# Kernel tuning notes

Measured on AMD Instinct MI355X. Metric: run time of the kernel, lower is better.

## Reference

```python
import jax, jax.numpy as jnp
import numpy as np

EPS = 1e-5
NEG = -1e9

def _ln(x, g, b):
    m = x.mean(-1, keepdims=True)
    v = ((x - m) ** 2).mean(-1, keepdims=True)
    return (x - m) / jnp.sqrt(v + EPS) * g + b

def setup_inputs() -> dict:
    key = jax.random.key(0)
    ks = jax.random.split(key, 32)
    B, N, D, F, L = 2, 512, 128, 512, 3
    s = 0.05
    rn = lambda k, sh, sc=s: jax.random.normal(k, sh, jnp.float32) * sc
    inp = {
        'rel_matrix': rn(ks[0], (B, N, N, 2), 1.0),
        'pre_w': rn(ks[1], (2, D)), 'pre_b': rn(ks[2], (D,)),
        'proj_w': rn(ks[3], (2 * D, D)), 'proj_b': rn(ks[4], (D,)),
        'out_w1': rn(ks[5], (D, D)),
        'bn_g': 1.0 + rn(ks[6], (D,)), 'bn_b': rn(ks[7], (D,)),
        'bn_m': rn(ks[8], (D,)),
        'bn_v': 0.5 + jax.random.uniform(ks[9], (D,), jnp.float32),
        'out_w2': rn(ks[10], (D, D)), 'out_b2': rn(ks[11], (D,)),
        'pe': rn(ks[12], (128, D)),
        'wq': rn(ks[13], (L, D, D)), 'bq': rn(ks[14], (L, D)),
        'wk': rn(ks[15], (L, D, D)), 'bk': rn(ks[16], (L, D)),
        'wv': rn(ks[17], (L, D, D)), 'bv': rn(ks[18], (L, D)),
        'wo': rn(ks[19], (L, D, D)), 'bo': rn(ks[20], (L, D)),
        'ln1g': jnp.ones((L, D), jnp.float32), 'ln1b': jnp.zeros((L, D), jnp.float32),
        'ln2g': jnp.ones((L, D), jnp.float32), 'ln2b': jnp.zeros((L, D), jnp.float32),
        'fw1': rn(ks[21], (L, D, F)), 'fb1': rn(ks[22], (L, F)),
        'fw2': rn(ks[23], (L, F, D)), 'fb2': rn(ks[24], (L, D)),
        'mask': jax.random.randint(ks[25], (B, N), 0, 2) > 0,
        'agent_id': jax.random.randint(ks[26], (B, N), 0, 128, dtype=jnp.int32),
    }
    return inp

def reference(rel_matrix, pre_w, pre_b, proj_w, proj_b, out_w1, bn_g, bn_b, bn_m, bn_v,
              out_w2, out_b2, pe, wq, bq, wk, bk, wv, bv, wo, bo,
              ln1g, ln1b, ln2g, ln2b, fw1, fb1, fw2, fb2, mask, agent_id):
    # --- pairwise relation chain (the headroom target) ---
    # symmetric pairwise validity mask (B,N,N)
    pm = (mask[:, None, :] & mask[:, :, None]).astype(rel_matrix.dtype)
    count = jnp.maximum(pm.sum(axis=2), 1.0)  # (B,N) valid-partner counts
    x = rel_matrix @ pre_w + pre_b            # (B,N,N,D) pre_proj Linear(2->128)
    pooled = jnp.einsum('bijd,bij->bid', x, pm) / count[..., None]  # masked mean over j
    x = jnp.concatenate([x, jnp.broadcast_to(pooled[:, :, None, :], x.shape)], axis=-1)
    x = x @ proj_w + proj_b                   # Linear(256->128)
    x = jnp.einsum('bijd,bij->bid', x, pm) / count[..., None]       # masked mean over j
    # out MLP: Linear(no bias) + BatchNorm1d(eval) + ReLU + Linear
    h = x @ out_w1
    h = (h - bn_m) / jnp.sqrt(bn_v + EPS) * bn_g + bn_b
    x = jax.nn.relu(h) @ out_w2 + out_b2
    x = x + pe[agent_id]                      # agent positional embedding
    # --- 3 post-norm single-head transformer layers (eval, dropout off) ---
    kbias = jnp.where(mask, 0.0, NEG)[:, None, :]  # key padding bias (B,1,N)
    scale = 1.0 / jnp.sqrt(jnp.asarray(x.shape[-1], x.dtype))
    for l in range(3):
        q = x @ wq[l] + bq[l]
        k = x @ wk[l] + bk[l]
        v = x @ wv[l] + bv[l]
        a = jax.nn.softmax(jnp.einsum('bid,bjd->bij', q, k) * scale + kbias, axis=-1)
        att = jnp.einsum('bij,bjd->bid', a, v) @ wo[l] + bo[l]
        x = _ln(x + att, ln1g[l], ln1b[l])
        ff = jax.nn.relu(x @ fw1[l] + fb1[l]) @ fw2[l] + fb2[l]
        x = _ln(x + ff, ln2g[l], ln2b[l])
    return x
```

## Files before the change

### kernel.cpp

```cpp
#include <hip/hip_runtime.h>
#include <hip/hip_bf16.h>

typedef unsigned short u16;
typedef unsigned int u32;
typedef unsigned char u8;
typedef __attribute__((ext_vector_type(8))) short bf16x8;
typedef __attribute__((ext_vector_type(4))) float f32x4;

#define DEV __device__ __forceinline__

DEV float bf2f(u16 u) { union { u32 i; float f; } c; c.i = ((u32)u) << 16; return c.f; }
DEV u16 f2bf(float f) {
  union { float f; u32 i; } c; c.f = f;
  u32 r = c.i + 0x7FFFu + ((c.i >> 16) & 1u);
  return (u16)(r >> 16);
}
DEV u32 pk2(float lo, float hi) { return (u32)f2bf(lo) | ((u32)f2bf(hi) << 16); }
DEV float rdsrc(const void* p, int e, int isb) {
  return isb ? bf2f(((const u16*)p)[e]) : ((const float*)p)[e];
}
DEV bf16x8 as_bf(uint4 v) { union { uint4 u; bf16x8 h; } c; c.u = v; return c.h; }

static constexpr int B = 2, N = 512, D = 128, F = 512;
static constexpr int NROW = B * N;
static constexpr float EPS = 1e-5f;
static constexpr float NEG = -1e9f;
static constexpr float SCALE = 0.08838834764831845f;

#define OFF_PRE_W   0
#define OFF_PRE_B   256
#define OFF_PROJ_B  33152
#define OFF_BN_G    49664
#define OFF_BN_B    49792
#define OFF_BN_M    49920
#define OFF_BN_V    50048
#define OFF_OUT_B2  66560
#define OFF_PE      66688
#define OFF_BQ      132224
#define OFF_BK      181760
#define OFF_BV      231296
#define OFF_BO      280832
#define OFF_LN1G    281216
#define OFF_LN1B    281600
#define OFF_LN2G    281984
#define OFF_LN2B    282368
#define OFF_FB1     479360
#define OFF_FB2     677504
#define W_TOTAL     677888

static constexpr int PB_PROJ = 0;
static constexpr int PB_OW1  = 8192;
static constexpr int PB_OW2  = 16384;
static constexpr int PB_L0   = 24576;
static constexpr int PB_LSTR = 98304;
static constexpr int PB_WO   = 24576;
static constexpr int PB_FW1  = 32768;
static constexpr int PB_FW2  = 65536;
static constexpr int PTOT    = 79872;

struct NEnt { const void* s; int off, n; };
struct PEnt { const void* s1; const void* s2; int o1, o2, dst, lgn, cum; };
struct PrepArgs { NEnt nrm[19]; PEnt pk[21]; };

template<int KT>
DEV f32x4 mmaKo(const uint4* __restrict__ aPk, const uint4* __restrict__ Bp,
                int ncol, int col, int lane, int kt0) {
  f32x4 acc = {0.f, 0.f, 0.f, 0.f};
  const int sub = lane >> 4;
  #pragma unroll
  for (int kt = 0; kt < KT; ++kt) {
    const int e8 = (kt0 + kt) * 4 + sub;
    acc = __builtin_amdgcn_mfma_f32_16x16x32_bf16(
        as_bf(aPk[e8 * 16 + (lane & 15)]),
        as_bf(Bp[(size_t)e8 * ncol + col]),
        acc, 0, 0, 0);
  }
  return acc;
}

template<int KT>
DEV void loadB(const uint4* __restrict__ Bp, int ncol, int col, int lane,
               int kt0, uint4* breg) {
  const int sub = lane >> 4;
  #pragma unroll
  for (int kt = 0; kt < KT; ++kt)
    breg[kt] = Bp[(size_t)((kt0 + kt) * 4 + sub) * ncol + col];
}

template<int KT>
DEV f32x4 mmaR(const uint4* __restrict__ aPk, const uint4* breg, int lane, int kt0) {
  f32x4 acc = {0.f, 0.f, 0.f, 0.f};
  const int sub = lane >> 4;
  #pragma unroll
  for (int kt = 0; kt < KT; ++kt) {
    const int e8 = (kt0 + kt) * 4 + sub;
    acc = __builtin_amdgcn_mfma_f32_16x16x32_bf16(
        as_bf(aPk[e8 * 16 + (lane & 15)]),
        as_bf(breg[kt]),
        acc, 0, 0, 0);
  }
  return acc;
}

DEV void packRD(u32* aPkU, int r, int d, float v) {
  const float p = __shfl_xor(v, 1, 64);
  if (!(d & 1))
    aPkU[(((d >> 3) * 16 + r) << 2) + ((d >> 1) & 3)] = pk2(v, p);
}

DEV void packP16(u32* aPkU, int colbase, int lane, f32x4 v) {
  f32x4 p;
  #pragma unroll
  for (int g = 0; g < 4; ++g) p[g] = __shfl_xor(v[g], 1, 64);
  if (!(lane & 1)) {
    const int c = colbase + lane;
    const int e8 = c >> 3, slot = (c >> 1) & 3;
    #pragma unroll
    for (int g = 0; g < 4; ++g)
      aPkU[((e8 * 16 + g) << 2) + slot] = pk2(v[g], p[g]);
  }
}

__global__ __launch_bounds__(256) void k_prep(PrepArgs pa,
    const void* __restrict__ bnv, const void* __restrict__ maskp,
    int* __restrict__ flags, int* __restrict__ mbuf,
    float* __restrict__ W, u32* __restrict__ Wb)
{
  const int t = threadIdx.x, bid = blockIdx.x;
  __shared__ int s_nb, s_m4, s_m2;
  if (t == 0) { s_nb = 0; s_m4 = 0; s_m2 = 0; }
  __syncthreads();
  if (t < 64) {
    const u32 w = ((const u32*)bnv)[t];
    if (((w >> 8) & 0xFFu) != 0x3Fu || ((w >> 24) & 0xFFu) != 0x3Fu)
      atomicOr(&s_nb, 1);
  }
  __syncthreads();
  const int isb = s_nb ? 0 : 1;

  if (bid < 16) {
    for (int ten = 0; ten < 19; ++ten) {
      const NEnt E = pa.nrm[ten];
      for (int e = bid * 256 + t; e < E.n; e += 16 * 256)
        W[E.off + e] = rdsrc(E.s, e, isb);
    }
  } else if (bid < 511) {
    for (int g = (bid - 16) * 256 + t; g < PTOT; g += 495 * 256) {
      int ei = 0;
      #pragma unroll
      for (int k = 1; k < 21; ++k) if (g >= pa.pk[k].cum) ei = k;
      const PEnt E = pa.pk[ei];
      const int li = g - E.cum;
      const int e8 = li >> E.lgn, c = li & ((1 << E.lgn) - 1);
      float f[8];
      #pragma unroll
      for (int i = 0; i < 8; ++i) {
        const int si = ((e8 * 8 + i) << E.lgn) + c;
        f[i] = rdsrc(E.s1, E.o1 + si, isb);
        if (E.s2) f[i] += rdsrc(E.s2, E.o2 + si, isb);
      }
      uint4 w;
      w.x = pk2(f[0], f[1]); w.y = pk2(f[2], f[3]);
      w.z = pk2(f[4], f[5]); w.w = pk2(f[6], f[7]);
      ((uint4*)(Wb + E.dst))[li] = w;
    }
  } else {
    {
      const u32 w = ((const u32*)maskp)[t];
      if (!(w == 0u || w == 1u || w == 0x3F800000u)) atomicOr(&s_m4, 1);
      if (!(w == 0u || w == 1u || w == 0x10000u || w == 0x10001u ||
            w == 0x3F80u || w == 0x3F800000u || w == 0x3F803F80u)) atomicOr(&s_m2, 1);
    }
    __syncthreads();
    const int mode = (!s_m4) ? 4 : ((!s_m2) ? 2 : 1);
    if (t == 0) { flags[0] = isb; flags[1] = mode; }
    #pragma unroll
    for (int k = 0; k < 4; ++k) {
      const int e = k * 256 + t;
      int v;
      if (mode == 4)      v = (((const u32*)maskp)[e] != 0u);
      else if (mode == 2) v = (((const u16*)maskp)[e] != 0);
      else                v = (((const u8*)maskp)[e]  != 0);
      mbuf[e] = v;
    }
  }
}

__global__ __launch_bounds__(512) void k_relq(
    const void* __restrict__ relv, const float* __restrict__ W,
    const u32* __restrict__ Wb,
    const int* __restrict__ flags, const int* __restrict__ mbuf,
    const int* __restrict__ agent_id, float* __restrict__ xbuf,
    u32* __restrict__ qP, u32* __restrict__ kbT, u32* __restrict__ vbT)
{
  const int t = threadIdx.x;
  const int blk = blockIdx.x;
  const int row0 = blk * 4;
  const int b = row0 >> 9;
  const int wid = t >> 6;
  const int lane = t & 63;

  __shared__ uint4 aPk[2][256];
  __shared__ float wred[8][9];
  __shared__ float sT0[4], sT1[4], sMt;

  u32* a0 = (u32*)&aPk[0][0];
  u32* a1 = (u32*)&aPk[1][0];

  float s0[4] = {0, 0, 0, 0}, s1[4] = {0, 0, 0, 0}, cnt;
  {
    const int j = t;
    const float m = (float)mbuf[b * N + j];
    cnt = m;
    if (flags[0]) {
      const u32* rel2 = (const u32*)relv;
      #pragma unroll
      for (int r = 0; r < 4; ++r) {
        const u32 u = rel2[(size_t)(row0 + r) * N + j];
        s0[r] += m * bf2f((u16)(u & 0xFFFFu));
        s1[r] += m * bf2f((u16)(u >> 16));
      }
    } else {
      const float2* relf = (const float2*)relv;
      #pragma unroll
      for (int r = 0; r < 4; ++r) {
        const float2 u = relf[(size_t)(row0 + r) * N + j];
        s0[r] += m * u.x; s1[r] += m * u.y;
      }
    }
  }
  if ((t & 15) >= 4) {
    const uint4 z = {0u, 0u, 0u, 0u};
    aPk[t >> 8][t & 255] = z;
  }
  #pragma unroll
  for (int o = 32; o > 0; o >>= 1) {
    #pragma unroll
    for (int r = 0; r < 4; ++r) {
      s0[r] += __shfl_xor(s0[r], o, 64);
      s1[r] += __shfl_xor(s1[r], o, 64);
    }
    cnt += __shfl_xor(cnt, o, 64);
  }
  if ((t & 63) == 0) {
    #pragma unroll
    for (int r = 0; r < 4; ++r) { wred[wid][r] = s0[r]; wred[wid][4 + r] = s1[r]; }
    wred[wid][8] = cnt;
  }
  __syncthreads();
  if (t < 4) {
    float a0v = 0, a1v = 0;
    #pragma unroll
    for (int w = 0; w < 8; ++w) { a0v += wred[w][t]; a1v += wred[w][4 + t]; }
    sT0[t] = a0v; sT1[t] = a1v;
  }
  if (t == 8) {
    float c = 0;
    #pragma unroll
    for (int w = 0; w < 8; ++w) c += wred[w][8];
    sMt = c;
  }
  __syncthreads();

  {
    const int r = t >> 7, c = t & 127;
    const int mi = mbuf[row0 + r];
    const float v = mi ? (sT0[r] * W[OFF_PRE_W + c] + sT1[r] * W[OFF_PRE_W + D + c]) / sMt
                         + W[OFF_PRE_B + c]
                       : 0.f;
    packRD(a0, r, c, v);
  }
  __syncthreads();

  {
    const int col = wid * 16 + (lane & 15);
    f32x4 acc = mmaKo<4>(&aPk[0][0], (const uint4*)(Wb + PB_PROJ), 128, col, lane, 0);
    if (lane < 16) {
      const float pb = W[OFF_PROJ_B + col];
      f32x4 v;
      #pragma unroll
      for (int g = 0; g < 4; ++g) v[g] = mbuf[row0 + g] ? acc[g] + pb : 0.f;
      packP16(a1, wid * 16, lane, v);
    }
  }
  __syncthreads();

  {
    const int col = wid * 16 + (lane & 15);
    f32x4 acc = mmaKo<4>(&aPk[1][0], (const uint4*)(Wb + PB_OW1), 128, col, lane, 0);
    if (lane < 16) {
      const float bnm = W[OFF_BN_M + col];
      const float rs  = __frsqrt_rn(W[OFF_BN_V + col] + EPS);
      const float bg  = W[OFF_BN_G + col], bb = W[OFF_BN_B + col];
      f32x4 v;
      #pragma unroll
      for (int g = 0; g < 4; ++g) v[g] = fmaxf((acc[g] - bnm) * rs * bg + bb, 0.f);
      packP16(a0, wid * 16, lane, v);
    }
  }
  __syncthreads();

  {
    const int col = wid * 16 + (lane & 15);
    f32x4 acc = mmaKo<4>(&aPk[0][0], (const uint4*)(Wb + PB_OW2), 128, col, lane, 0);
    if (lane < 16) {
      const float ob = W[OFF_OUT_B2 + col];
      f32x4 v;
      #pragma unroll
      for (int g = 0; g < 4; ++g) {
        const int aid = agent_id[row0 + g];
        v[g] = acc[g] + ob + W[OFF_PE + aid * D + col];
        xbuf[(size_t)(row0 + g) * D + col] = v[g];
      }
      packP16(a1, wid * 16, lane, v);
    }
  }
  __syncthreads();

  {
    const int col = wid * 16 + (lane & 15);
    const int i0 = row0 & 511;
    #pragma unroll
    for (int m = 0; m < 3; ++m) {
      f32x4 acc = mmaKo<4>(&aPk[1][0], (const uint4*)(Wb + PB_L0 + m * 8192), 128, col, lane, 0);
      if (lane < 16) {
        const float bb = W[(m == 0 ? OFF_BQ : m == 1 ? OFF_BK : OFF_BV) + col];
        f32x4 v;
        #pragma unroll
        for (int g = 0; g < 4; ++g) v[g] = acc[g] + bb;
        if (m == 0) {
          f32x4 p;
          #pragma unroll
          for (int g = 0; g < 4; ++g) p[g] = __shfl_xor(v[g], 1, 64);
          if (!(lane & 1)) {
            const int e8 = col >> 3, slot = (col >> 1) & 3;
            #pragma unroll
            for (int g = 0; g < 4; ++g)
              qP[blk * 256 + (e8 * 4 + g) * 4 + slot] = pk2(v[g], p[g]);
          }
        } else if (m == 1) {
          f32x4 p;
          #pragma unroll
          for (int g = 0; g < 4; ++g) p[g] = __shfl_xor(v[g], 1, 64);
          if (!(lane & 1)) {
            const int e8 = col >> 3, slot = (col >> 1) & 3;
            #pragma unroll
            for (int g = 0; g < 4; ++g)
              ((u32*)kbT)[(((size_t)b * 16 + e8) * 512 + i0 + g) * 4 + slot]
                  = pk2(v[g] * SCALE, p[g] * SCALE);
          }
        } else {
          uint2 w;
          w.x = pk2(v[0], v[1]); w.y = pk2(v[2], v[3]);
          *(uint2*)(vbT + (((size_t)b * 64 + (i0 >> 3)) * 128 + col) * 4 + 2 * ((i0 >> 2) & 1)) = w;
        }
      }
    }
  }
}

__global__ __launch_bounds__(1024) void k_layer(
    const u32* __restrict__ qPin, const u32* __restrict__ kinT, const u32* __restrict__ vinT,
    const float* __restrict__ W, const u32* __restrict__ Wb, const int l, const int last,
    u32* __restrict__ qPout, u32* __restrict__ koutT, u32* __restrict__ voutT,
    const int* __restrict__ mbuf, float* __restrict__ xbuf, float* __restrict__ outp)
{
  const int t = threadIdx.x;
  const int blk = blockIdx.x;
  const int row0 = blk * 4;
  const int b = row0 >> 9;
  const int wid = t >> 6;
  const int lane = t & 63;
  const int w8 = wid & 7, half = wid >> 3;

  const uint4* WOp = (const uint4*)(Wb + PB_L0 + l * PB_LSTR + PB_WO);
  const uint4* W1p = (const uint4*)(Wb + PB_L0 + l * PB_LSTR + PB_FW1);
  const uint4* W2p = (const uint4*)(Wb + PB_L0 + l * PB_LSTR + PB_FW2);
  const float* bo  = W + OFF_BO  + l * D;
  const float* g1  = W + OFF_LN1G + l * D;
  const float* b1  = W + OFF_LN1B + l * D;
  const float* fb1 = W + OFF_FB1 + l * F;
  const float* fb2 = W + OFF_FB2 + l * D;
  const float* g2  = W + OFF_LN2G + l * D;
  const float* b2v = W + OFF_LN2B + l * D;

  __shared__ float bufA[4][512];
  __shared__ float xs[4][D];
  __shared__ float pA[4][D], pB[4][D];
  __shared__ uint4 aPk[2][1024];
  __shared__ float den[4];

  u32* a0 = (u32*)&aPk[0][0];
  u32* a1 = (u32*)&aPk[1][0];

  for (int i = t; i < 2048; i += 1024)
    if ((i & 15) >= 4) {
      const uint4 z = {0u, 0u, 0u, 0u};
      aPk[i >> 10][i & 1023] = z;
    }
  if (t < 64)
    aPk[0][(t >> 2) * 16 + (t & 3)] = ((const uint4*)qPin)[blk * 64 + t];
  const uint4* Kp = (const uint4*)kinT + (size_t)b * 16 * 512;
  uint4 kB[2][4];
  #pragma unroll
  for (int ii = 0; ii < 2; ++ii)
    loadB<4>(Kp, 512, (wid + 16 * ii) * 16 + (lane & 15), lane, 0, kB[ii]);
  __syncthreads();

  {
    #pragma unroll
    for (int ii = 0; ii < 2; ++ii) {
      const int col = (wid + 16 * ii) * 16 + (lane & 15);
      f32x4 acc = mmaR<4>(&aPk[0][0], kB[ii], lane, 0);
      if (lane < 16) {
        const float bias = mbuf[b * N + col] ? 0.f : NEG;
        #pragma unroll
        for (int g = 0; g < 4; ++g) bufA[g][col] = acc[g] + bias;
      }
    }
  }
  const uint4* Vp = (const uint4*)vinT + (size_t)b * 64 * 128;
  uint4 vB[8];
  loadB<8>(Vp, 128, w8 * 16 + (lane & 15), lane, half * 8, vB);
  __syncthreads();

  if (wid < 4) {
    const int r = wid;
    float pv[8];
    float mx = -1e30f;
    #pragma unroll
    for (int k = 0; k < 8; ++k) { pv[k] = bufA[r][lane + 64 * k]; mx = fmaxf(mx, pv[k]); }
    #pragma unroll
    for (int o = 32; o > 0; o >>= 1) mx = fmaxf(mx, __shfl_xor(mx, o, 64));
    float sum = 0.f;
    #pragma unroll
    for (int k = 0; k < 8; ++k) { pv[k] = __expf(pv[k] - mx); sum += pv[k]; }
    #pragma unroll
    for (int o = 32; o > 0; o >>= 1) sum += __shfl_xor(sum, o, 64);
    #pragma unroll
    for (int k = 0; k < 8; ++k) {
      const float pp = __shfl_xor(pv[k], 1, 64);
      if (!(lane & 1)) {
        const int c = lane + 64 * k;
        a1[(((c >> 3) * 16 + r) << 2) + ((c >> 1) & 3)] = pk2(pv[k], pp);
      }
    }
    if (lane == 0) den[r] = sum;
  }
  __syncthreads();

  {
    const int col = w8 * 16 + (lane & 15);
    f32x4 acc = mmaR<8>(&aPk[1][0], vB, lane, half * 8);
    if (lane < 16) {
      float* dst = half ? &pB[0][0] : &pA[0][0];
      #pragma unroll
      for (int g = 0; g < 4; ++g) dst[g * D + col] = acc[g];
    }
  }
  uint4 woB[2];
  loadB<2>(WOp, 128, w8 * 16 + (lane & 15), lane, half * 2, woB);
  __syncthreads();

  if (t < 512) {
    const int r = t >> 7, d = t & 127;
    packRD(a0, r, d, (pA[r][d] + pB[r][d]) / den[r]);
  }
  __syncthreads();

  {
    const int col = w8 * 16 + (lane & 15);
    f32x4 acc = mmaR<2>(&aPk[0][0], woB, lane, half * 2);
    if (lane < 16) {
      float* dst = half ? &pB[0][0] : &pA[0][0];
      #pragma unroll
      for (int g = 0; g < 4; ++g) dst[g * D + col] = acc[g];
    }
  }
  uint4 w1B[2][4];
  #pragma unroll
  for (int ii = 0; ii < 2; ++ii)
    loadB<4>(W1p, 512, (wid + 16 * ii) * 16 + (lane & 15), lane, 0, w1B[ii]);
  __syncthreads();

  if (wid < 4) {
    const int r = wid;
    float tv[2];
    #pragma unroll
    for (int k = 0; k < 2; ++k) {
      const int d = lane + 64 * k;
      tv[k] = pA[r][d] + pB[r][d] + bo[d] + xbuf[(size_t)(row0 + r) * D + d];
    }
    float s = tv[0] + tv[1], sq = tv[0] * tv[0] + tv[1] * tv[1];
    #pragma unroll
    for (int o = 32; o > 0; o >>= 1) { s += __shfl_xor(s, o, 64); sq += __shfl_xor(sq, o, 64); }
    const float mean = s * (1.f / 128.f);
    const float var  = sq * (1.f / 128.f) - mean * mean;
    const float rstd = __frsqrt_rn(var + EPS);
    #pragma unroll
    for (int k = 0; k < 2; ++k) {
      const int d = lane + 64 * k;
      const float xn = (tv[k] - mean) * rstd * g1[d] + b1[d];
      xs[r][d] = xn;
      const float pp = __shfl_xor(xn, 1, 64);
      if (!(lane & 1))
        a1[(((d >> 3) * 16 + r) << 2) + ((d >> 1) & 3)] = pk2(xn, pp);
    }
  }
  __syncthreads();

  {
    #pragma unroll
    for (int ii = 0; ii < 2; ++ii) {
      const int colbase = (wid + 16 * ii) * 16;
      f32x4 acc = mmaR<4>(&aPk[1][0], w1B[ii], lane, 0);
      if (lane < 16) {
        const float bb = fb1[colbase + lane];
        f32x4 v;
        #pragma unroll
        for (int g = 0; g < 4; ++g) v[g] = fmaxf(acc[g] + bb, 0.f);
        packP16(a0, colbase, lane, v);
      }
    }
  }
  uint4 w2B[8];
  loadB<8>(W2p, 128, w8 * 16 + (lane & 15), lane, half * 8, w2B);
  __syncthreads();

  {
    const int col = w8 * 16 + (lane & 15);
    f32x4 acc = mmaR<8>(&aPk[0][0], w2B, lane, half * 8);
    if (lane < 16) {
      float* dst = half ? &pB[0][0] : &pA[0][0];
      #pragma unroll
      for (int g = 0; g < 4; ++g) dst[g * D + col] = acc[g];
    }
  }
  uint4 jB[2][4];
  if (!last) {
    #pragma unroll
    for (int it = 0; it < 2; ++it) {
      const int task = wid + 16 * it;
      if (task < 24) {
        const int m = task >> 3, c8 = task & 7;
        const uint4* Bp = (const uint4*)(Wb + PB_L0 + (l + 1) * PB_LSTR + m * 8192);
        loadB<4>(Bp, 128, c8 * 16 + (lane & 15), lane, 0, jB[it]);
      }
    }
  }
  __syncthreads();

  if (wid < 4) {
    const int r = wid;
    float tv[2];
    #pragma unroll
    for (int k = 0; k < 2; ++k) {
      const int d = lane + 64 * k;
      tv[k] = pA[r][d] + pB[r][d] + fb2[d] + xs[r][d];
    }
    float s = tv[0] + tv[1], sq = tv[0] * tv[0] + tv[1] * tv[1];
    #pragma unroll
    for (int o = 32; o > 0; o >>= 1) { s += __shfl_xor(s, o, 64); sq += __shfl_xor(sq, o, 64); }
    const float mean = s * (1.f / 128.f);
    const float var  = sq * (1.f / 128.f) - mean * mean;
    const float rstd = __frsqrt_rn(var + EPS);
    #pragma unroll
    for (int k = 0; k < 2; ++k) {
      const int d = lane + 64 * k;
      const float xn = (tv[k] - mean) * rstd * g2[d] + b2v[d];
      xbuf[(size_t)(row0 + r) * D + d] = xn;
      if (last) outp[(size_t)(row0 + r) * D + d] = xn;
      const float pp = __shfl_xor(xn, 1, 64);
      if (!last && !(lane & 1))
        a1[(((d >> 3) * 16 + r) << 2) + ((d >> 1) & 3)] = pk2(xn, pp);
    }
  }

  if (!last) {
    __syncthreads();
    const int i0 = row0 & 511;
    #pragma unroll
    for (int it = 0; it < 2; ++it) {
      const int task = wid + 16 * it;
      if (task < 24) {
        const int m = task >> 3, c8 = task & 7;
        const int col = c8 * 16 + (lane & 15);
        f32x4 acc = mmaR<4>(&aPk[1][0], jB[it], lane, 0);
        if (lane < 16) {
          const float bb = W[(m == 0 ? OFF_BQ : m == 1 ? OFF_BK : OFF_BV) + (l + 1) * D + col];
          f32x4 v;
          #pragma unroll
          for (int g = 0; g < 4; ++g) v[g] = acc[g] + bb;
          if (m == 0) {
            f32x4 p;
            #pragma unroll
            for (int g = 0; g < 4; ++g) p[g] = __shfl_xor(v[g], 1, 64);
            if (!(lane & 1)) {
              const int e8 = col >> 3, slot = (col >> 1) & 3;
              #pragma unroll
              for (int g = 0; g < 4; ++g)
                qPout[blk * 256 + (e8 * 4 + g) * 4 + slot] = pk2(v[g], p[g]);
            }
          } else if (m == 1) {
            f32x4 p;
            #pragma unroll
            for (int g = 0; g < 4; ++g) p[g] = __shfl_xor(v[g], 1, 64);
            if (!(lane & 1)) {
              const int e8 = col >> 3, slot = (col >> 1) & 3;
              #pragma unroll
              for (int g = 0; g < 4; ++g)
                ((u32*)koutT)[(((size_t)b * 16 + e8) * 512 + i0 + g) * 4 + slot]
                    = pk2(v[g] * SCALE, p[g] * SCALE);
            }
          } else {
            uint2 w;
            w.x = pk2(v[0], v[1]); w.y = pk2(v[2], v[3]);
            *(uint2*)(voutT + (((size_t)b * 64 + (i0 >> 3)) * 128 + col) * 4 + 2 * ((i0 >> 2) & 1)) = w;
          }
        }
      }
    }
  }
}

extern "C" void kernel_launch(void* const* d_in, const int* in_sizes, int n_in,
                              void* d_out, int out_size, void* d_ws, size_t ws_size,
                              hipStream_t stream) {
  int*   flags = (int*)d_ws;
  int*   mbuf  = flags + 16;
  float* xbuf  = (float*)d_ws + 1040;
  u32*   qP0   = (u32*)(xbuf + NROW * D);
  u32*   qP1   = qP0 + 65536;
  u32*   kT0   = qP1 + 65536;
  u32*   kT1   = kT0 + 65536;
  u32*   vT0   = kT1 + 65536;
  u32*   vT1   = vT0 + 65536;
  float* W     = (float*)(vT1 + 65536);
  u32*   Wb    = (u32*)(W + W_TOTAL);

  PrepArgs pa;
  {
    const NEnt nrm[19] = {
      {d_in[1],  OFF_PRE_W,  256}, {d_in[2],  OFF_PRE_B, 128},
      {d_in[4],  OFF_PROJ_B, 128},
      {d_in[6],  OFF_BN_G,   128}, {d_in[7],  OFF_BN_B,  128},
      {d_in[8],  OFF_BN_M,   128}, {d_in[9],  OFF_BN_V,  128},
      {d_in[11], OFF_OUT_B2, 128}, {d_in[12], OFF_PE,  16384},
      {d_in[14], OFF_BQ,     384}, {d_in[16], OFF_BK,    384},
      {d_in[18], OFF_BV,     384}, {d_in[20], OFF_BO,    384},
      {d_in[21], OFF_LN1G,   384}, {d_in[22], OFF_LN1B,  384},
      {d_in[23], OFF_LN2G,   384}, {d_in[24], OFF_LN2B,  384},
      {d_in[26], OFF_FB1,   1536}, {d_in[28], OFF_FB2,   384}};
    for (int i = 0; i < 19; ++i) pa.nrm[i] = nrm[i];

    pa.pk[0] = {d_in[3], d_in[3], 0, 16384, PB_PROJ, 7, 0};
    pa.pk[1] = {d_in[5],  nullptr, 0, 0, PB_OW1, 7, 2048};
    pa.pk[2] = {d_in[10], nullptr, 0, 0, PB_OW2, 7, 4096};
    for (int l = 0; l < 3; ++l) {
      const int lb = PB_L0 + l * PB_LSTR;
      const int cl = 6144 + l * 24576;
      pa.pk[3 + 6 * l + 0] = {d_in[13], nullptr, l * 16384, 0, lb,          7, cl};
      pa.pk[3 + 6 * l + 1] = {d_in[15], nullptr, l * 16384, 0, lb + 8192,   7, cl + 2048};
      pa.pk[3 + 6 * l + 2] = {d_in[17], nullptr, l * 16384, 0, lb + 16384,  7, cl + 4096};
      pa.pk[3 + 6 * l + 3] = {d_in[19], nullptr, l * 16384, 0, lb + PB_WO,  7, cl + 6144};
      pa.pk[3 + 6 * l + 4] = {d_in[25], nullptr, l * 65536, 0, lb + PB_FW1, 9, cl + 8192};
      pa.pk[3 + 6 * l + 5] = {d_in[27], nullptr, l * 65536, 0, lb + PB_FW2, 7, cl + 16384};
    }
  }
  const int* agent_id = (const int*)d_in[30];

  k_prep<<<512, 256, 0, stream>>>(pa, d_in[9], d_in[29], flags, mbuf, W, Wb);
  k_relq<<<NROW / 4, 512, 0, stream>>>(d_in[0], W, Wb, flags, mbuf, agent_id, xbuf,
                                       qP0, kT0, vT0);

  u32* qs_[2] = {qP0, qP1};
  u32* ks_[2] = {kT0, kT1};
  u32* vs_[2] = {vT0, vT1};
  for (int l = 0; l < 3; ++l) {
    const int cur = l & 1, nxt = cur ^ 1;
    const int last = (l == 2);
    k_layer<<<NROW / 4, 1024, 0, stream>>>(
        qs_[cur], ks_[cur], vs_[cur],
        W, Wb, l, last,
        qs_[nxt], ks_[nxt], vs_[nxt],
        mbuf, xbuf, last ? (float*)d_out : (float*)nullptr);
  }
}
```

Measured before the change: 63.11 us.

## Spread weight packing across later kernels to overlap with compute

The prep kernel now packs only the pre-layer weights and layer-0 QKV, and shrinks its grid to 256 blocks. Each later kernel packs the weights needed by the following stage: relq packs layer-0 WO/FFN plus layer-1 QKV, and each layer kernel packs the next layer's weights. This moves the large bf16 repacking off the critical path of the first kernel and overlaps it with compute. In exchange every downstream kernel gains extra global traffic and instructions at its start, and each kernel now writes buffers that the next launch reads, which relies on stream ordering.

Result: slower. 68.73 us (+8.9%).

```diff
diff --git a/kernel.cpp b/kernel.cpp
--- a/kernel.cpp
+++ b/kernel.cpp
@@ -56,11 +56,34 @@
 static constexpr int PB_WO   = 24576;
 static constexpr int PB_FW1  = 32768;
 static constexpr int PB_FW2  = 65536;
-static constexpr int PTOT    = 79872;
 
 struct NEnt { const void* s; int off, n; };
 struct PEnt { const void* s1; const void* s2; int o1, o2, dst, lgn, cum; };
-struct PrepArgs { NEnt nrm[19]; PEnt pk[21]; };
+struct PrepArgs { NEnt nrm[19]; PEnt pk[6]; };
+struct PackSet { PEnt e[6]; int n, total; };
+
+DEV void doPack(const PackSet& ps, int isb, u32* __restrict__ Wb,
+                int gbase, int gstride) {
+  for (int g = gbase; g < ps.total; g += gstride) {
+    int ei = 0;
+    #pragma unroll
+    for (int k = 1; k < 6; ++k) if (k < ps.n && g >= ps.e[k].cum) ei = k;
+    const PEnt E = ps.e[ei];
+    const int li = g - E.cum;
+    const int e8 = li >> E.lgn, c = li & ((1 << E.lgn) - 1);
+    float f[8];
+    #pragma unroll
+    for (int i = 0; i < 8; ++i) {
+      const int si = ((e8 * 8 + i) << E.lgn) + c;
+      f[i] = rdsrc(E.s1, E.o1 + si, isb);
+      if (E.s2) f[i] += rdsrc(E.s2, E.o2 + si, isb);
+    }
+    uint4 w;
+    w.x = pk2(f[0], f[1]); w.y = pk2(f[2], f[3]);
+    w.z = pk2(f[4], f[5]); w.w = pk2(f[6], f[7]);
+    ((uint4*)(Wb + E.dst))[li] = w;
+  }
+}
 
 template<int KT>
 DEV f32x4 mmaKo(const uint4* __restrict__ aPk, const uint4* __restrict__ Bp,
@@ -144,26 +167,12 @@
       for (int e = bid * 256 + t; e < E.n; e += 16 * 256)
         W[E.off + e] = rdsrc(E.s, e, isb);
     }
-  } else if (bid < 511) {
-    for (int g = (bid - 16) * 256 + t; g < PTOT; g += 495 * 256) {
-      int ei = 0;
-      #pragma unroll
-      for (int k = 1; k < 21; ++k) if (g >= pa.pk[k].cum) ei = k;
-      const PEnt E = pa.pk[ei];
-      const int li = g - E.cum;
-      const int e8 = li >> E.lgn, c = li & ((1 << E.lgn) - 1);
-      float f[8];
-      #pragma unroll
-      for (int i = 0; i < 8; ++i) {
-        const int si = ((e8 * 8 + i) << E.lgn) + c;
-        f[i] = rdsrc(E.s1, E.o1 + si, isb);
-        if (E.s2) f[i] += rdsrc(E.s2, E.o2 + si, isb);
-      }
-      uint4 w;
-      w.x = pk2(f[0], f[1]); w.y = pk2(f[2], f[3]);
-      w.z = pk2(f[4], f[5]); w.w = pk2(f[6], f[7]);
-      ((uint4*)(Wb + E.dst))[li] = w;
-    }
+  } else if (bid < 255) {
+    PackSet ps;
+    #pragma unroll
+    for (int k = 0; k < 6; ++k) ps.e[k] = pa.pk[k];
+    ps.n = 6; ps.total = 12288;
+    doPack(ps, isb, Wb, (bid - 16) * 256 + t, 239 * 256);
   } else {
     {
       const u32 w = ((const u32*)maskp)[t];
@@ -188,7 +197,7 @@
 
 __global__ __launch_bounds__(512) void k_relq(
     const void* __restrict__ relv, const float* __restrict__ W,
-    const u32* __restrict__ Wb,
+    u32* __restrict__ Wb, PackSet ps,
     const int* __restrict__ flags, const int* __restrict__ mbuf,
     const int* __restrict__ agent_id, float* __restrict__ xbuf,
     u32* __restrict__ qP, u32* __restrict__ kbT, u32* __restrict__ vbT)
@@ -206,6 +215,8 @@
 
   u32* a0 = (u32*)&aPk[0][0];
   u32* a1 = (u32*)&aPk[1][0];
+
+  doPack(ps, flags[0], Wb, blk * 512 + t, 256 * 512);
 
   float s0[4] = {0, 0, 0, 0}, s1[4] = {0, 0, 0, 0}, cnt;
   {
@@ -361,9 +372,11 @@
 
 __global__ __launch_bounds__(1024) void k_layer(
     const u32* __restrict__ qPin, const u32* __restrict__ kinT, const u32* __restrict__ vinT,
-    const float* __restrict__ W, const u32* __restrict__ Wb, const int l, const int last,
+    const float* __restrict__ W, u32* __restrict__ Wb, PackSet ps,
+    const int l, const int last,
     u32* __restrict__ qPout, u32* __restrict__ koutT, u32* __restrict__ voutT,
-    const int* __restrict__ mbuf, float* __restrict__ xbuf, float* __restrict__ outp)
+    const int* __restrict__ flags, const int* __restrict__ mbuf,
+    float* __restrict__ xbuf, float* __restrict__ outp)
 {
   const int t = threadIdx.x;
   const int blk = blockIdx.x;
@@ -392,6 +405,8 @@
 
   u32* a0 = (u32*)&aPk[0][0];
   u32* a1 = (u32*)&aPk[1][0];
+
+  doPack(ps, flags[0], Wb, blk * 1024 + t, 256 * 1024);
 
   for (int i = t; i < 2048; i += 1024)
     if ((i & 15) >= 4) {
@@ -656,33 +671,50 @@
     pa.pk[0] = {d_in[3], d_in[3], 0, 16384, PB_PROJ, 7, 0};
     pa.pk[1] = {d_in[5],  nullptr, 0, 0, PB_OW1, 7, 2048};
     pa.pk[2] = {d_in[10], nullptr, 0, 0, PB_OW2, 7, 4096};
-    for (int l = 0; l < 3; ++l) {
-      const int lb = PB_L0 + l * PB_LSTR;
-      const int cl = 6144 + l * 24576;
-      pa.pk[3 + 6 * l + 0] = {d_in[13], nullptr, l * 16384, 0, lb,          7, cl};
-      pa.pk[3 + 6 * l + 1] = {d_in[15], nullptr, l * 16384, 0, lb + 8192,   7, cl + 2048};
-      pa.pk[3 + 6 * l + 2] = {d_in[17], nullptr, l * 16384, 0, lb + 16384,  7, cl + 4096};
-      pa.pk[3 + 6 * l + 3] = {d_in[19], nullptr, l * 16384, 0, lb + PB_WO,  7, cl + 6144};
-      pa.pk[3 + 6 * l + 4] = {d_in[25], nullptr, l * 65536, 0, lb + PB_FW1, 9, cl + 8192};
-      pa.pk[3 + 6 * l + 5] = {d_in[27], nullptr, l * 65536, 0, lb + PB_FW2, 7, cl + 16384};
-    }
-  }
+    pa.pk[3] = {d_in[13], nullptr, 0, 0, PB_L0,          7, 6144};
+    pa.pk[4] = {d_in[15], nullptr, 0, 0, PB_L0 + 8192,   7, 8192};
+    pa.pk[5] = {d_in[17], nullptr, 0, 0, PB_L0 + 16384,  7, 10240};
+  }
+
+  auto mkLayerSet = [&](int l, bool withQKVnext) {
+    PackSet ps{};
+    const int lb = PB_L0 + l * PB_LSTR;
+    ps.e[0] = {d_in[19], nullptr, l * 16384, 0, lb + PB_WO,  7, 0};
+    ps.e[1] = {d_in[25], nullptr, l * 65536, 0, lb + PB_FW1, 9, 2048};
+    ps.e[2] = {d_in[27], nullptr, l * 65536, 0, lb + PB_FW2, 7, 10240};
+    if (withQKVnext) {
+      const int nb = PB_L0 + (l + 1) * PB_LSTR;
+      ps.e[3] = {d_in[13], nullptr, (l + 1) * 16384, 0, nb,         7, 18432};
+      ps.e[4] = {d_in[15], nullptr, (l + 1) * 16384, 0, nb + 8192,  7, 20480};
+      ps.e[5] = {d_in[17], nullptr, (l + 1) * 16384, 0, nb + 16384, 7, 22528};
+      ps.n = 6; ps.total = 24576;
+    } else {
+      ps.n = 3; ps.total = 18432;
+    }
+    return ps;
+  };
+  PackSet psRelq = mkLayerSet(0, true);
+  PackSet psL0   = mkLayerSet(1, true);
+  PackSet psL1   = mkLayerSet(2, false);
+  PackSet psL2{}; psL2.n = 0; psL2.total = 0;
+
   const int* agent_id = (const int*)d_in[30];
 
-  k_prep<<<512, 256, 0, stream>>>(pa, d_in[9], d_in[29], flags, mbuf, W, Wb);
-  k_relq<<<NROW / 4, 512, 0, stream>>>(d_in[0], W, Wb, flags, mbuf, agent_id, xbuf,
-                                       qP0, kT0, vT0);
+  k_prep<<<256, 256, 0, stream>>>(pa, d_in[9], d_in[29], flags, mbuf, W, Wb);
+  k_relq<<<NROW / 4, 512, 0, stream>>>(d_in[0], W, Wb, psRelq, flags, mbuf,
+                                       agent_id, xbuf, qP0, kT0, vT0);
 
   u32* qs_[2] = {qP0, qP1};
   u32* ks_[2] = {kT0, kT1};
   u32* vs_[2] = {vT0, vT1};
+  PackSet psL[3] = {psL0, psL1, psL2};
   for (int l = 0; l < 3; ++l) {
     const int cur = l & 1, nxt = cur ^ 1;
     const int last = (l == 2);
     k_layer<<<NROW / 4, 1024, 0, stream>>>(
         qs_[cur], ks_[cur], vs_[cur],
-        W, Wb, l, last,
+        W, Wb, psL[l], l, last,
         qs_[nxt], ks_[nxt], vs_[nxt],
-        mbuf, xbuf, last ? (float*)d_out : (float*)nullptr);
-  }
-}
+        flags, mbuf, xbuf, last ? (float*)d_out : (float*)nullptr);
+  }
+}
```

## Defer packing of later-stage weights into extra blocks of the relation kernel

Applied to the files above, without the earlier changes.

The prep kernel now packs only the weights k_relq needs (proj, out MLP, layer-0 QKV) and launches half as many blocks. Packing of Wo/FFN weights and layer 1-2 QKV moves into 64 extra blocks appended to k_relq, so that work runs alongside the pairwise relation computation instead of ahead of it. This shortens the serial prep stage. The extra blocks compete with the main k_relq blocks for CUs and bandwidth.

New measurement: 63.65 us. No clear change (+0.9%).

```diff
diff --git a/kernel.cpp b/kernel.cpp
--- a/kernel.cpp
+++ b/kernel.cpp
@@ -56,11 +56,33 @@
 static constexpr int PB_WO   = 24576;
 static constexpr int PB_FW1  = 32768;
 static constexpr int PB_FW2  = 65536;
-static constexpr int PTOT    = 79872;
 
 struct NEnt { const void* s; int off, n; };
 struct PEnt { const void* s1; const void* s2; int o1, o2, dst, lgn, cum; };
-struct PrepArgs { NEnt nrm[19]; PEnt pk[21]; };
+struct PrepArgs { NEnt nrm[19]; PEnt pk[6]; };
+struct PackAll { PEnt e[15]; int total; };
+
+DEV void doPackAll(const PackAll& ps, int isb, u32* __restrict__ Wb,
+                   int gbase, int gstride) {
+  for (int g = gbase; g < ps.total; g += gstride) {
+    int ei = 0;
+    #pragma unroll
+    for (int k = 1; k < 15; ++k) if (g >= ps.e[k].cum) ei = k;
+    const PEnt E = ps.e[ei];
+    const int li = g - E.cum;
+    const int e8 = li >> E.lgn, c = li & ((1 << E.lgn) - 1);
+    float f[8];
+    #pragma unroll
+    for (int i = 0; i < 8; ++i) {
+      const int si = ((e8 * 8 + i) << E.lgn) + c;
+      f[i] = rdsrc(E.s1, E.o1 + si, isb);
+    }
+    uint4 w;
+    w.x = pk2(f[0], f[1]); w.y = pk2(f[2], f[3]);
+    w.z = pk2(f[4], f[5]); w.w = pk2(f[6], f[7]);
+    ((uint4*)(Wb + E.dst))[li] = w;
+  }
+}
 
 template<int KT>
 DEV f32x4 mmaKo(const uint4* __restrict__ aPk, const uint4* __restrict__ Bp,
@@ -144,11 +166,11 @@
       for (int e = bid * 256 + t; e < E.n; e += 16 * 256)
         W[E.off + e] = rdsrc(E.s, e, isb);
     }
-  } else if (bid < 511) {
-    for (int g = (bid - 16) * 256 + t; g < PTOT; g += 495 * 256) {
+  } else if (bid < 255) {
+    for (int g = (bid - 16) * 256 + t; g < 12288; g += 239 * 256) {
       int ei = 0;
       #pragma unroll
-      for (int k = 1; k < 21; ++k) if (g >= pa.pk[k].cum) ei = k;
+      for (int k = 1; k < 6; ++k) if (g >= pa.pk[k].cum) ei = k;
       const PEnt E = pa.pk[ei];
       const int li = g - E.cum;
       const int e8 = li >> E.lgn, c = li & ((1 << E.lgn) - 1);
@@ -188,13 +210,19 @@
 
 __global__ __launch_bounds__(512) void k_relq(
     const void* __restrict__ relv, const float* __restrict__ W,
-    const u32* __restrict__ Wb,
+    u32* __restrict__ Wb, PackAll psAll,
     const int* __restrict__ flags, const int* __restrict__ mbuf,
     const int* __restrict__ agent_id, float* __restrict__ xbuf,
     u32* __restrict__ qP, u32* __restrict__ kbT, u32* __restrict__ vbT)
 {
   const int t = threadIdx.x;
   const int blk = blockIdx.x;
+
+  if (blk >= 256) {
+    doPackAll(psAll, flags[0], Wb, (blk - 256) * 512 + t, 64 * 512);
+    return;
+  }
+
   const int row0 = blk * 4;
   const int b = row0 >> 9;
   const int wid = t >> 6;
@@ -656,22 +684,34 @@
     pa.pk[0] = {d_in[3], d_in[3], 0, 16384, PB_PROJ, 7, 0};
     pa.pk[1] = {d_in[5],  nullptr, 0, 0, PB_OW1, 7, 2048};
     pa.pk[2] = {d_in[10], nullptr, 0, 0, PB_OW2, 7, 4096};
+    pa.pk[3] = {d_in[13], nullptr, 0, 0, PB_L0,          7, 6144};
+    pa.pk[4] = {d_in[15], nullptr, 0, 0, PB_L0 + 8192,   7, 8192};
+    pa.pk[5] = {d_in[17], nullptr, 0, 0, PB_L0 + 16384,  7, 10240};
+  }
+
+  PackAll psAll;
+  {
+    int cum = 0, i = 0;
     for (int l = 0; l < 3; ++l) {
       const int lb = PB_L0 + l * PB_LSTR;
-      const int cl = 6144 + l * 24576;
-      pa.pk[3 + 6 * l + 0] = {d_in[13], nullptr, l * 16384, 0, lb,          7, cl};
-      pa.pk[3 + 6 * l + 1] = {d_in[15], nullptr, l * 16384, 0, lb + 8192,   7, cl + 2048};
-      pa.pk[3 + 6 * l + 2] = {d_in[17], nullptr, l * 16384, 0, lb + 16384,  7, cl + 4096};
-      pa.pk[3 + 6 * l + 3] = {d_in[19], nullptr, l * 16384, 0, lb + PB_WO,  7, cl + 6144};
-      pa.pk[3 + 6 * l + 4] = {d_in[25], nullptr, l * 65536, 0, lb + PB_FW1, 9, cl + 8192};
-      pa.pk[3 + 6 * l + 5] = {d_in[27], nullptr, l * 65536, 0, lb + PB_FW2, 7, cl + 16384};
-    }
-  }
+      psAll.e[i++] = {d_in[19], nullptr, l * 16384, 0, lb + PB_WO,  7, cum}; cum += 2048;
+      psAll.e[i++] = {d_in[25], nullptr, l * 65536, 0, lb + PB_FW1, 9, cum}; cum += 8192;
+      psAll.e[i++] = {d_in[27], nullptr, l * 65536, 0, lb + PB_FW2, 7, cum}; cum += 8192;
+    }
+    for (int l = 1; l < 3; ++l) {
+      const int nb = PB_L0 + l * PB_LSTR;
+      psAll.e[i++] = {d_in[13], nullptr, l * 16384, 0, nb,         7, cum}; cum += 2048;
+      psAll.e[i++] = {d_in[15], nullptr, l * 16384, 0, nb + 8192,  7, cum}; cum += 2048;
+      psAll.e[i++] = {d_in[17], nullptr, l * 16384, 0, nb + 16384, 7, cum}; cum += 2048;
+    }
+    psAll.total = cum;
+  }
+
   const int* agent_id = (const int*)d_in[30];
 
-  k_prep<<<512, 256, 0, stream>>>(pa, d_in[9], d_in[29], flags, mbuf, W, Wb);
-  k_relq<<<NROW / 4, 512, 0, stream>>>(d_in[0], W, Wb, flags, mbuf, agent_id, xbuf,
-                                       qP0, kT0, vT0);
+  k_prep<<<256, 256, 0, stream>>>(pa, d_in[9], d_in[29], flags, mbuf, W, Wb);
+  k_relq<<<320, 512, 0, stream>>>(d_in[0], W, Wb, psAll, flags, mbuf,
+                                  agent_id, xbuf, qP0, kT0, vT0);
 
   u32* qs_[2] = {qP0, qP1};
   u32* ks_[2] = {kT0, kT1};
```
